# Performance work log

Measured on AMD Instinct MI355X. Metric: run time of the kernel, lower is better.

## Reference

```python
import jax, jax.numpy as jnp
import numpy as np

NEG_INF = -9e15
ALPHA = 0.2  # attention leaky_relu slope


def _gat_layer(h, adj_mask, W, a1, a2):
    # h: [N, Fin], W: [Fin, D], a1/a2: [D]
    Wh = h @ W                                   # [N, D]
    f1 = Wh @ a1                                 # [N]
    f2 = Wh @ a2                                 # [N]
    e = jax.nn.leaky_relu(f1[:, None] + f2[None, :], ALPHA)  # [N, N]
    scores = jnp.where(adj_mask, e, NEG_INF)
    att = jax.nn.softmax(scores, axis=-1)        # row-normalized over neighbors
    return att @ Wh                              # [N, D]


def setup_inputs() -> dict:
    key = jax.random.key(0)
    ks = jax.random.split(key, 12)
    N, Fin, H, D, C = 4096, 512, 8, 64, 64
    s = 0.1
    x = jax.random.normal(ks[0], (N, Fin), jnp.float32)
    adj = jax.random.randint(ks[1], (N, N), 0, 2, jnp.int32)
    W = jax.random.normal(ks[2], (H, Fin, D), jnp.float32) * s
    a1 = jax.random.normal(ks[3], (H, D), jnp.float32) * s
    a2 = jax.random.normal(ks[4], (H, D), jnp.float32) * s
    Wo = jax.random.normal(ks[5], (H * D, C), jnp.float32) * s
    ao1 = jax.random.normal(ks[6], (C,), jnp.float32) * s
    ao2 = jax.random.normal(ks[7], (C,), jnp.float32) * s
    W1 = jax.random.normal(ks[8], (512, N), jnp.float32) * 0.01  # nn.Linear(N, 512)
    b1 = jnp.zeros((512,), jnp.float32)
    W2 = jax.random.normal(ks[9], (256, 512), jnp.float32) * 0.04  # nn.Linear(512, 256)
    b2 = jnp.zeros((256,), jnp.float32)
    return {"x": x, "adj": adj, "W": W, "a1": a1, "a2": a2,
            "Wo": Wo, "ao1": ao1, "ao2": ao2,
            "W1": W1, "b1": b1, "W2": W2, "b2": b2}


def reference(x, adj, W, a1, a2, Wo, ao1, ao2, W1, b1, W2, b2):
    mask = adj > 0                                    # [N, N]
    # multi-head dense attention, concat=True -> ELU per head
    heads = jax.vmap(lambda Wk, a1k, a2k: _gat_layer(x, mask, Wk, a1k, a2k))(W, a1, a2)  # [H, N, D]
    h = jax.nn.elu(heads).transpose(1, 0, 2).reshape(x.shape[0], -1)  # [N, H*D]
    # output attention layer, concat=False (no inner ELU), then outer ELU
    out = jax.nn.elu(_gat_layer(h, mask, Wo, ao1, ao2))  # [N, C]
    out = jax.nn.log_softmax(out, axis=0)                # over nodes (dim=0)
    # MLP head on transposed features: [C, N] -> [C, 512] -> [C, 256]
    y = jax.nn.leaky_relu(out.T @ W1.T + b1, 0.1)
    y = y @ W2.T + b2
    return y
```

## Files before the change

### kernel.cpp

```cpp
#include <hip/hip_runtime.h>
#include <hip/hip_bf16.h>
#include <math.h>


#define N_NODES 4096
#define FIN 512
#define NHEAD 8
#define DHEAD 64
#define NCLS 64
#define NW 64

typedef unsigned short u16;
typedef unsigned long long u64;
typedef __attribute__((ext_vector_type(8))) short bf16x8;
typedef __attribute__((ext_vector_type(4))) float f32x4;

__device__ __forceinline__ float lrelu02(float x) { return x > 0.f ? x : 0.2f * x; }
__device__ __forceinline__ u16 bf16u(float x) {
    __hip_bfloat16 h = __float2bfloat16(x);
    return __builtin_bit_cast(unsigned short, h);
}
__device__ __forceinline__ f32x4 mfma16(bf16x8 a, bf16x8 b, f32x4 c) {
    return __builtin_amdgcn_mfma_f32_16x16x32_bf16(a, b, c, 0, 0, 0);
}
__device__ __forceinline__ unsigned fkey(float f) {
    unsigned u = __builtin_bit_cast(unsigned, f);
    return (u & 0x80000000u) ? ~u : (u | 0x80000000u);
}
__device__ __forceinline__ float funkey(unsigned k) {
    unsigned u = (k & 0x80000000u) ? (k ^ 0x80000000u) : ~k;
    return __builtin_bit_cast(float, u);
}

__global__ __launch_bounds__(256) void prep(
    const int* __restrict__ adj, u64* __restrict__ mb, unsigned* __restrict__ gmk,
    const float* __restrict__ x, u16* __restrict__ xB,
    const float* __restrict__ W1, u16* __restrict__ W1B,
    const float* __restrict__ W, const float* __restrict__ Wo,
    u16* __restrict__ WBt, u16* __restrict__ WoBt) {
    __shared__ alignas(16) u16 T[64][72];
    const int bid = blockIdx.x, t = threadIdx.x;
    if (bid < 1024) {
        if (bid == 0 && t < 16) gmk[t] = 0u;
        int nwaves = (1024 * 256) >> 6;
        int wid = (bid * 256 + t) >> 6;
        int lane = t & 63;
        for (int w = wid; w < N_NODES * NW; w += nwaves) {
            int i = w >> 6, wc = w & 63;
            int j = (wc << 6) | lane;
            u64 m = __ballot(adj[(size_t)i * N_NODES + j] > 0);
            if (lane == 0) mb[w] = m;
        }
    } else if (bid < 5120) {
        int i = (bid - 1024) * 256 + t;
        const float* s;
        u16* d;
        if (i < N_NODES * FIN / 4) { s = x; d = xB; }
        else { i -= N_NODES * FIN / 4; s = W1; d = W1B; }
        float4 v = ((const float4*)s)[i];
        ushort4 o = {bf16u(v.x), bf16u(v.y), bf16u(v.z), bf16u(v.w)};
        ((ushort4*)d)[i] = o;
    } else {
        int idx = bid - 5120;
        int y = idx >> 3, xb = idx & 7;
        const float* src = (y < 8) ? W + (size_t)y * FIN * DHEAD : Wo;
        u16* d = (y < 8) ? WBt + (size_t)y * DHEAD * FIN : WoBt;
        const int j0 = xb * 64;
        const int row = t & 63, g = t >> 6;
        #pragma unroll
        for (int k = 0; k < 16; k += 4) {
            float4 v = *(const float4*)(src + (size_t)(j0 + row) * 64 + g * 16 + k);
            T[g * 16 + k + 0][row] = bf16u(v.x);
            T[g * 16 + k + 1][row] = bf16u(v.y);
            T[g * 16 + k + 2][row] = bf16u(v.z);
            T[g * 16 + k + 3][row] = bf16u(v.w);
        }
        __syncthreads();
        const int dd = t >> 2, jc = (t & 3) * 16;
        *(uint4*)(d + (size_t)dd * FIN + j0 + jc) = *(const uint4*)&T[dd][jc];
        *(uint4*)(d + (size_t)dd * FIN + j0 + jc + 8) = *(const uint4*)&T[dd][jc + 8];
    }
}

__global__ __launch_bounds__(256) void gemm_fused(
    const u16* __restrict__ A, int lda, const u16* __restrict__ Bt, int ldb,
    const float* __restrict__ a1a, const float* __restrict__ a2a,
    u16* __restrict__ WhBT, float* __restrict__ f1o, float* __restrict__ f2o,
    unsigned* __restrict__ gmk, int K) {
    __shared__ alignas(16) u16 T[64][72];
    const int t = threadIdx.x, lane = t & 63, wv = t >> 6;
    const int c16 = lane & 15, kg = lane >> 4;
    const int h = blockIdx.x;
    const int bm = blockIdx.y * 64;
    const u16* Ap = A + (size_t)(bm + wv * 16 + c16) * lda + kg * 8;
    const u16* Bp = Bt + (size_t)(h * 64 + c16) * ldb + kg * 8;
    f32x4 acc[4] = {};
    #pragma unroll 4
    for (int k0 = 0; k0 < K; k0 += 32) {
        bf16x8 a = *(const bf16x8*)(Ap + k0);
        #pragma unroll
        for (int ct = 0; ct < 4; ++ct) {
            bf16x8 b = *(const bf16x8*)(Bp + (size_t)ct * 16 * ldb + k0);
            acc[ct] = mfma16(a, b, acc[ct]);
        }
    }
    float a1v[4], a2v[4];
    #pragma unroll
    for (int ct = 0; ct < 4; ++ct) {
        a1v[ct] = a1a[h * 64 + ct * 16 + c16];
        a2v[ct] = a2a[h * 64 + ct * 16 + c16];
    }
    float mx = -1e30f;
    #pragma unroll
    for (int r = 0; r < 4; ++r) {
        float s1 = 0.f, s2 = 0.f;
        int rl = wv * 16 + kg * 4 + r;
        #pragma unroll
        for (int ct = 0; ct < 4; ++ct) {
            float v = acc[ct][r];
            s1 = fmaf(v, a1v[ct], s1);
            s2 = fmaf(v, a2v[ct], s2);
            T[ct * 16 + c16][rl] = bf16u(v);
        }
        #pragma unroll
        for (int off = 1; off < 16; off <<= 1) {
            s1 += __shfl_xor(s1, off, 64);
            s2 += __shfl_xor(s2, off, 64);
        }
        if (c16 == 0) {
            f1o[(size_t)h * N_NODES + bm + rl] = s1;
            f2o[(size_t)h * N_NODES + bm + rl] = s2;
        }
        mx = fmaxf(mx, s2);
    }
    mx = fmaxf(mx, __shfl_xor(mx, 16, 64));
    mx = fmaxf(mx, __shfl_xor(mx, 32, 64));
    if (lane == 0) atomicMax(&gmk[h], fkey(mx));
    __syncthreads();
    const int dd = t >> 2, jc = (t & 3) * 16;
    u16* dst = WhBT + (size_t)(h * 64 + dd) * N_NODES + bm;
    *(uint4*)(dst + jc) = *(const uint4*)&T[dd][jc];
    *(uint4*)(dst + jc + 8) = *(const uint4*)&T[dd][jc + 8];
}

__global__ void coefk(const float* __restrict__ f1, const float* __restrict__ f2,
                      const unsigned* __restrict__ gmk, float4* __restrict__ rowc,
                      float2* __restrict__ uv) {
    int h = blockIdx.y;
    int i = blockIdx.x * 256 + threadIdx.x;
    float g = funkey(gmk[h]);
    float a = f1[(size_t)h * N_NODES + i];
    float s = a + g;
    float M = lrelu02(s);
    rowc[(size_t)h * N_NODES + i] = make_float4(__expf(s - M), __expf(0.2f * s - M), 0.f, 0.f);
    float b = f2[(size_t)h * N_NODES + i] - g;
    uv[(size_t)h * N_NODES + i] = make_float2(__expf(b), __expf(0.2f * b));
}

template <int NH, int ROWS, int JSPLIT, int OUTF>
__global__ __launch_bounds__(256) void attn_v3(
    const u16* __restrict__ WhB, const float2* __restrict__ uv,
    const float4* __restrict__ rowc, const u64* __restrict__ mb,
    float* __restrict__ outp, float* __restrict__ denP) {
    constexpr int NQ = ROWS / 4;
    constexpr int NMT = ROWS / 16;
    constexpr int NJT = (N_NODES / 64) / JSPLIT;
    __shared__ alignas(16) u16 pS[2][ROWS][64];
    __shared__ float Tof[(OUTF == 3) ? 64 * (ROWS + 1) : 1];
    const int b = blockIdx.x;
    int h, ib, js;
    if (NH == 8) { h = b & 7; int r = b >> 3; js = r % JSPLIT; ib = r / JSPLIT; }
    else { h = 0; js = b % JSPLIT; ib = b / JSPLIT; }
    const int i0 = ib * ROWS;
    const int jt0 = js * NJT;
    const int t = threadIdx.x, lane = t & 63, wv = t >> 6;
    const int wv_u = __builtin_amdgcn_readfirstlane(wv);

    const float2* __restrict__ uvp = uv + (size_t)h * N_NODES;
    const float4* __restrict__ rcp = rowc + (size_t)h * N_NODES;
    const u64* __restrict__ mbp = mb + (size_t)(i0 + wv_u) * NW + jt0;

    float Aq[NQ], Bq[NQ], den[NQ];
    #pragma unroll
    for (int q = 0; q < NQ; ++q) {
        float4 rc = rcp[i0 + q * 4 + wv];
        Aq[q] = rc.x; Bq[q] = rc.y; den[q] = 0.f;
    }
    const int wcE = lane ^ (wv << 3);
    const int wcO = lane ^ ((wv + 4) << 3);
    const int kg = lane >> 4, c16 = lane & 15;
    const int ocol = wv * 16 + c16;
    const u16* bptr = WhB + ((size_t)h * 64 + ocol) * N_NODES + jt0 * 64 + kg * 8;
    const int sw8 = (c16 & 7) << 3;
    f32x4 acc[NMT] = {};

    bf16x8 b0 = *(const bf16x8*)(bptr);
    bf16x8 b1 = *(const bf16x8*)(bptr + 32);
    float2 uvv = uvp[jt0 * 64 + lane];
    u64 m[NQ];
    #pragma unroll
    for (int q = 0; q < NQ; ++q) m[q] = mbp[q * 4 * NW];

    for (int it = 0; it < NJT; ++it) {
        const int buf = it & 1;
        const int nit = (it + 1 < NJT) ? it + 1 : it;
        bf16x8 nb0 = *(const bf16x8*)(bptr + (size_t)nit * 64);
        bf16x8 nb1 = *(const bf16x8*)(bptr + (size_t)nit * 64 + 32);
        float2 nuv = uvp[(jt0 + nit) * 64 + lane];
        u64 nm[NQ];
        #pragma unroll
        for (int q = 0; q < NQ; ++q) nm[q] = mbp[q * 4 * NW + nit];
        #pragma unroll
        for (int q = 0; q < NQ; ++q) {
            unsigned wlo = __builtin_amdgcn_readfirstlane((unsigned)m[q]);
            unsigned whi = __builtin_amdgcn_readfirstlane((unsigned)(m[q] >> 32));
            u64 ws = ((u64)whi << 32) | wlo;
            float tv = fmaxf(Aq[q] * uvv.x, Bq[q] * uvv.y);
            float p;
            asm("v_cndmask_b32 %0, 0, %1, %2" : "=v"(p) : "v"(tv), "s"(ws));
            den[q] += p;
            pS[buf][q * 4 + wv][(q & 1) ? wcO : wcE] = bf16u(p);
        }
        __syncthreads();
        __builtin_amdgcn_s_setprio(1);
        #pragma unroll
        for (int mt = 0; mt < NMT; ++mt) {
            const u16* ap = &pS[buf][mt * 16 + c16][0];
            bf16x8 a0 = *(const bf16x8*)&ap[(kg * 8) ^ sw8];
            bf16x8 a1 = *(const bf16x8*)&ap[(32 + kg * 8) ^ sw8];
            acc[mt] = mfma16(a0, b0, acc[mt]);
            acc[mt] = mfma16(a1, b1, acc[mt]);
        }
        __builtin_amdgcn_s_setprio(0);
        b0 = nb0; b1 = nb1; uvv = nuv;
        #pragma unroll
        for (int q = 0; q < NQ; ++q) m[q] = nm[q];
    }

    #pragma unroll
    for (int q = 0; q < NQ; ++q) {
        float s = den[q];
        #pragma unroll
        for (int off = 32; off; off >>= 1) s += __shfl_xor(s, off, 64);
        den[q] = s;
    }

    if constexpr (OUTF == 1) {
        if (lane == 0) {
            #pragma unroll
            for (int q = 0; q < NQ; ++q)
                denP[(size_t)js * (8 * N_NODES) + (size_t)h * N_NODES + i0 + q * 4 + wv] = den[q];
        }
        float* dst = outp + (size_t)js * N_NODES * 512;
        #pragma unroll
        for (int mt = 0; mt < NMT; ++mt)
            #pragma unroll
            for (int r = 0; r < 4; ++r)
                dst[(size_t)(i0 + mt * 16 + kg * 4 + r) * 512 + h * 64 + ocol] = acc[mt][r];
    } else {
        if (lane == 0) {
            #pragma unroll
            for (int q = 0; q < NQ; ++q)
                denP[(size_t)js * N_NODES + i0 + q * 4 + wv] = den[q];
        }
        #pragma unroll
        for (int mt = 0; mt < NMT; ++mt)
            #pragma unroll
            for (int r = 0; r < 4; ++r)
                Tof[ocol * (ROWS + 1) + mt * 16 + kg * 4 + r] = acc[mt][r];
        __syncthreads();
        const int c = t >> 2, r0 = (t & 3) * 8;
        float* dst = outp + (size_t)js * 64 * N_NODES + (size_t)c * N_NODES + i0 + r0;
        float4 v0 = {Tof[c * (ROWS + 1) + r0 + 0], Tof[c * (ROWS + 1) + r0 + 1],
                     Tof[c * (ROWS + 1) + r0 + 2], Tof[c * (ROWS + 1) + r0 + 3]};
        float4 v1 = {Tof[c * (ROWS + 1) + r0 + 4], Tof[c * (ROWS + 1) + r0 + 5],
                     Tof[c * (ROWS + 1) + r0 + 6], Tof[c * (ROWS + 1) + r0 + 7]};
        *(float4*)(dst) = v0;
        *(float4*)(dst + 4) = v1;
    }
}

__global__ __launch_bounds__(256) void combine8(
    const float* __restrict__ part, const float* __restrict__ denp,
    u16* __restrict__ hB) {
    const int t4 = (blockIdx.x * 256 + threadIdx.x) * 4;
    const int i = t4 >> 9, c = t4 & 511, h = c >> 6;
    float4 p0 = *(const float4*)(part + t4);
    float4 p1 = *(const float4*)(part + (size_t)N_NODES * 512 + t4);
    float d = denp[h * N_NODES + i] + denp[8 * N_NODES + h * N_NODES + i];
    float inv = d > 0.f ? 1.f / d : 0.f;
    float v[4] = {(p0.x + p1.x) * inv, (p0.y + p1.y) * inv,
                  (p0.z + p1.z) * inv, (p0.w + p1.w) * inv};
    ushort4 o;
    #pragma unroll
    for (int k = 0; k < 4; ++k) {
        float e = v[k] > 0.f ? v[k] : expm1f(v[k]);
        ((u16*)&o)[k] = bf16u(e);
    }
    *(ushort4*)(hB + t4) = o;
}

__global__ __launch_bounds__(256) void combine1_lsm(
    const float* __restrict__ partT, const float* __restrict__ denp,
    u16* __restrict__ lsT) {
    __shared__ float vb[N_NODES];
    __shared__ float r[256];
    const int c = blockIdx.x, t = threadIdx.x;
    float m = -1e30f;
    for (int i = t * 4; i < N_NODES; i += 1024) {
        float4 s = {0.f, 0.f, 0.f, 0.f}, d = {0.f, 0.f, 0.f, 0.f};
        #pragma unroll
        for (int js = 0; js < 4; ++js) {
            float4 pv = *(const float4*)(partT + (size_t)js * 64 * N_NODES +
                                         (size_t)c * N_NODES + i);
            float4 dv = *(const float4*)(denp + (size_t)js * N_NODES + i);
            s.x += pv.x; s.y += pv.y; s.z += pv.z; s.w += pv.w;
            d.x += dv.x; d.y += dv.y; d.z += dv.z; d.w += dv.w;
        }
        float vv[4] = {d.x > 0.f ? s.x / d.x : 0.f, d.y > 0.f ? s.y / d.y : 0.f,
                       d.z > 0.f ? s.z / d.z : 0.f, d.w > 0.f ? s.w / d.w : 0.f};
        #pragma unroll
        for (int k = 0; k < 4; ++k) {
            float e = vv[k] > 0.f ? vv[k] : expm1f(vv[k]);
            vb[i + k] = e;
            m = fmaxf(m, e);
        }
    }
    r[t] = m;
    __syncthreads();
    for (int s = 128; s; s >>= 1) {
        if (t < s) r[t] = fmaxf(r[t], r[t + s]);
        __syncthreads();
    }
    m = r[0];
    __syncthreads();
    float sum = 0.f;
    for (int i = t; i < N_NODES; i += 256) sum += __expf(vb[i] - m);
    r[t] = sum;
    __syncthreads();
    for (int s = 128; s; s >>= 1) {
        if (t < s) r[t] += r[t + s];
        __syncthreads();
    }
    float lse = m + __logf(r[0]);
    for (int i = t * 4; i < N_NODES; i += 1024) {
        ushort4 o = {bf16u(vb[i] - lse), bf16u(vb[i + 1] - lse),
                     bf16u(vb[i + 2] - lse), bf16u(vb[i + 3] - lse)};
        *(ushort4*)(lsT + (size_t)c * N_NODES + i) = o;
    }
}

__global__ __launch_bounds__(256) void mlp1_mfma(
    const u16* __restrict__ lsT, const u16* __restrict__ W1B,
    float* __restrict__ part) {
    const int t = threadIdx.x, lane = t & 63, wv = t >> 6;
    const int c16 = lane & 15, kg = lane >> 4;
    const int ks = blockIdx.x & 15;
    const int bn = (blockIdx.x >> 4) * 64;
    const int kb = ks * 256;
    const u16* Ap = lsT + (size_t)(wv * 16 + c16) * N_NODES + kb + kg * 8;
    const u16* Bp = W1B + (size_t)(bn + c16) * N_NODES + kb + kg * 8;
    f32x4 acc[4] = {};
    #pragma unroll
    for (int k0 = 0; k0 < 256; k0 += 32) {
        bf16x8 a = *(const bf16x8*)(Ap + k0);
        #pragma unroll
        for (int ct = 0; ct < 4; ++ct) {
            bf16x8 b = *(const bf16x8*)(Bp + (size_t)ct * 16 * N_NODES + k0);
            acc[ct] = mfma16(a, b, acc[ct]);
        }
    }
    float* dst = part + (size_t)ks * 64 * 512;
    #pragma unroll
    for (int ct = 0; ct < 4; ++ct)
        #pragma unroll
        for (int r = 0; r < 4; ++r)
            dst[(size_t)(wv * 16 + kg * 4 + r) * 512 + bn + ct * 16 + c16] = acc[ct][r];
}

__global__ __launch_bounds__(256) void mlp2f(
    const float* __restrict__ part, const float* __restrict__ b1,
    const float* __restrict__ W2, const float* __restrict__ b2,
    float* __restrict__ out) {
    __shared__ alignas(16) float row[512];
    const int c = blockIdx.x, t = threadIdx.x;
    #pragma unroll
    for (int half = 0; half < 2; ++half) {
        int o = t + half * 256;
        float s = 0.f;
        #pragma unroll
        for (int ks = 0; ks < 16; ++ks)
            s += part[(size_t)ks * 32768 + (size_t)c * 512 + o];
        s += b1[o];
        row[o] = s > 0.f ? s : 0.1f * s;
    }
    __syncthreads();
    float acc = 0.f;
    #pragma unroll 4
    for (int o = 0; o < 512; o += 4) {
        float4 w4 = *(const float4*)(W2 + (size_t)t * 512 + o);
        float4 r4 = *(const float4*)(&row[o]);
        acc += w4.x * r4.x + w4.y * r4.y + w4.z * r4.z + w4.w * r4.w;
    }
    out[(size_t)c * 256 + t] = acc + b2[t];
}

extern "C" void kernel_launch(void* const* d_in, const int* in_sizes, int n_in,
                              void* d_out, int out_size, void* d_ws, size_t ws_size,
                              hipStream_t stream) {
    const float* x   = (const float*)d_in[0];
    const int*   adj = (const int*)d_in[1];
    const float* W   = (const float*)d_in[2];
    const float* a1  = (const float*)d_in[3];
    const float* a2  = (const float*)d_in[4];
    const float* Wo  = (const float*)d_in[5];
    const float* ao1 = (const float*)d_in[6];
    const float* ao2 = (const float*)d_in[7];
    const float* W1  = (const float*)d_in[8];
    const float* b1  = (const float*)d_in[9];
    const float* W2  = (const float*)d_in[10];
    const float* b2  = (const float*)d_in[11];
    float* out = (float*)d_out;

    char* ws = (char*)d_ws;
    size_t off = 0;
    auto alloc = [&](size_t bytes) {
        void* p = ws + off;
        off += (bytes + 255) & ~(size_t)255;
        return p;
    };
    u64*     mb     = (u64*)alloc((size_t)N_NODES * NW * 8);
    u16*     xB     = (u16*)alloc((size_t)N_NODES * FIN * 2);
    u16*     WBt    = (u16*)alloc((size_t)NHEAD * DHEAD * FIN * 2);
    u16*     WoBt   = (u16*)alloc((size_t)DHEAD * FIN * 2);
    u16*     W1B    = (u16*)alloc((size_t)512 * N_NODES * 2);
    u16*     WhB    = (u16*)alloc((size_t)NHEAD * DHEAD * N_NODES * 2);
    u16*     WhoB   = (u16*)alloc((size_t)DHEAD * N_NODES * 2);
    u16*     hB     = (u16*)alloc((size_t)N_NODES * 512 * 2);
    float*   part8  = (float*)alloc((size_t)2 * N_NODES * 512 * 4);
    float*   den8   = (float*)alloc((size_t)2 * 8 * N_NODES * 4);
    float*   f1b    = (float*)alloc((size_t)9 * N_NODES * 4);
    float*   f2b    = (float*)alloc((size_t)9 * N_NODES * 4);
    unsigned* gmk   = (unsigned*)alloc(16 * 4);
    float4*  rowc   = (float4*)alloc((size_t)9 * N_NODES * 16);
    float2*  uvb    = (float2*)alloc((size_t)9 * N_NODES * 8);
    char*    ov     = (char*)part8;
    float*   partT1 = (float*)(ov);
    float*   den1   = (float*)(ov + ((size_t)4 << 20));
    u16*     lsT    = (u16*)(ov + ((size_t)4 << 20) + (256 << 10));
    float*   part   = (float*)(ov + ((size_t)5 << 20));
    (void)ws_size; (void)in_sizes; (void)n_in; (void)out_size;

    prep<<<5192, 256, 0, stream>>>(adj, mb, gmk, x, xB, W1, W1B, W, Wo, WBt, WoBt);
    gemm_fused<<<dim3(8, 64), 256, 0, stream>>>(xB, FIN, WBt, FIN, a1, a2,
                                                WhB, f1b, f2b, gmk, FIN);
    coefk<<<dim3(16, 8), 256, 0, stream>>>(f1b, f2b, gmk, rowc, uvb);
    attn_v3<8, 64, 2, 1><<<(N_NODES / 64) * 2 * 8, 256, 0, stream>>>(
        WhB, uvb, rowc, mb, part8, den8);
    combine8<<<N_NODES * 512 / 4 / 256, 256, 0, stream>>>(part8, den8, hB);
    gemm_fused<<<dim3(1, 64), 256, 0, stream>>>(hB, 512, WoBt, FIN, ao1, ao2,
                                                WhoB, f1b + (size_t)8 * N_NODES,
                                                f2b + (size_t)8 * N_NODES, gmk + 8, FIN);
    coefk<<<dim3(16, 1), 256, 0, stream>>>(f1b + (size_t)8 * N_NODES,
                                           f2b + (size_t)8 * N_NODES, gmk + 8,
                                           rowc + (size_t)8 * N_NODES,
                                           uvb + (size_t)8 * N_NODES);
    attn_v3<1, 32, 4, 3><<<(N_NODES / 32) * 4, 256, 0, stream>>>(
        WhoB, uvb + (size_t)8 * N_NODES, rowc + (size_t)8 * N_NODES, mb, partT1, den1);
    combine1_lsm<<<64, 256, 0, stream>>>(partT1, den1, lsT);
    mlp1_mfma<<<128, 256, 0, stream>>>(lsT, W1B, part);
    mlp2f<<<64, 256, 0, stream>>>(part, b1, W2, b2, out);
}
```

Baseline: 201.4 us.

## Unroll attention loop by two, store head partials in bf16, split output layer wider

The attention main loop is unrolled by two with named A/B register sets, so prefetches of the next tile's Wh, uv and mask words are interleaved explicitly with the P-fill and MFMA phases. The multi-head partial outputs are now stored as bf16 instead of fp32, which halves the write and read traffic between attn_v3 and combine8. The output-layer attention uses JSPLIT 8 instead of 4 to launch more blocks, and the workspace is enlarged into a 16MB pool to hold the extra partials. In exchange, the bf16 partial sums lose precision, and NJT must now be even for the unrolled loop to be correct (it is 32 and 8 here).

After: 217.2 us. +7.8%, slower.

```diff
diff --git a/kernel.cpp b/kernel.cpp
--- a/kernel.cpp
+++ b/kernel.cpp
@@ -19,6 +19,10 @@
 __device__ __forceinline__ u16 bf16u(float x) {
     __hip_bfloat16 h = __float2bfloat16(x);
     return __builtin_bit_cast(unsigned short, h);
+}
+__device__ __forceinline__ float b2f(u16 v) {
+    unsigned u = (unsigned)v << 16;
+    return __builtin_bit_cast(float, u);
 }
 __device__ __forceinline__ f32x4 mfma16(bf16x8 a, bf16x8 b, f32x4 c) {
     return __builtin_amdgcn_mfma_f32_16x16x32_bf16(a, b, c, 0, 0, 0);
@@ -161,7 +165,7 @@
 __global__ __launch_bounds__(256) void attn_v3(
     const u16* __restrict__ WhB, const float2* __restrict__ uv,
     const float4* __restrict__ rowc, const u64* __restrict__ mb,
-    float* __restrict__ outp, float* __restrict__ denP) {
+    void* __restrict__ outp, float* __restrict__ denP) {
     constexpr int NQ = ROWS / 4;
     constexpr int NMT = ROWS / 16;
     constexpr int NJT = (N_NODES / 64) / JSPLIT;
@@ -194,47 +198,60 @@
     const int sw8 = (c16 & 7) << 3;
     f32x4 acc[NMT] = {};
 
-    bf16x8 b0 = *(const bf16x8*)(bptr);
-    bf16x8 b1 = *(const bf16x8*)(bptr + 32);
-    float2 uvv = uvp[jt0 * 64 + lane];
-    u64 m[NQ];
-    #pragma unroll
-    for (int q = 0; q < NQ; ++q) m[q] = mbp[q * 4 * NW];
-
-    for (int it = 0; it < NJT; ++it) {
-        const int buf = it & 1;
-        const int nit = (it + 1 < NJT) ? it + 1 : it;
-        bf16x8 nb0 = *(const bf16x8*)(bptr + (size_t)nit * 64);
-        bf16x8 nb1 = *(const bf16x8*)(bptr + (size_t)nit * 64 + 32);
-        float2 nuv = uvp[(jt0 + nit) * 64 + lane];
-        u64 nm[NQ];
-        #pragma unroll
-        for (int q = 0; q < NQ; ++q) nm[q] = mbp[q * 4 * NW + nit];
+    bf16x8 bA0, bA1, bB0, bB1;
+    float2 uvA, uvB;
+    u64 mA[NQ], mB[NQ];
+
+    auto pfB = [&](int nit, bf16x8& x0, bf16x8& x1, float2& u) {
+        x0 = *(const bf16x8*)(bptr + (size_t)nit * 64);
+        x1 = *(const bf16x8*)(bptr + (size_t)nit * 64 + 32);
+        u = uvp[(jt0 + nit) * 64 + lane];
+    };
+    auto pfM = [&](int nit, u64* mm) {
+        #pragma unroll
+        for (int q = 0; q < NQ; ++q) mm[q] = mbp[q * 4 * NW + nit];
+    };
+    auto pph = [&](int bufI, const u64* mm, float2 u) {
         #pragma unroll
         for (int q = 0; q < NQ; ++q) {
-            unsigned wlo = __builtin_amdgcn_readfirstlane((unsigned)m[q]);
-            unsigned whi = __builtin_amdgcn_readfirstlane((unsigned)(m[q] >> 32));
+            unsigned wlo = __builtin_amdgcn_readfirstlane((unsigned)mm[q]);
+            unsigned whi = __builtin_amdgcn_readfirstlane((unsigned)(mm[q] >> 32));
             u64 ws = ((u64)whi << 32) | wlo;
-            float tv = fmaxf(Aq[q] * uvv.x, Bq[q] * uvv.y);
+            float tv = fmaxf(Aq[q] * u.x, Bq[q] * u.y);
             float p;
             asm("v_cndmask_b32 %0, 0, %1, %2" : "=v"(p) : "v"(tv), "s"(ws));
             den[q] += p;
-            pS[buf][q * 4 + wv][(q & 1) ? wcO : wcE] = bf16u(p);
-        }
-        __syncthreads();
+            pS[bufI][q * 4 + wv][(q & 1) ? wcO : wcE] = bf16u(p);
+        }
+    };
+    auto mm8 = [&](int bufI, bf16x8 v0, bf16x8 v1) {
         __builtin_amdgcn_s_setprio(1);
         #pragma unroll
         for (int mt = 0; mt < NMT; ++mt) {
-            const u16* ap = &pS[buf][mt * 16 + c16][0];
+            const u16* ap = &pS[bufI][mt * 16 + c16][0];
             bf16x8 a0 = *(const bf16x8*)&ap[(kg * 8) ^ sw8];
             bf16x8 a1 = *(const bf16x8*)&ap[(32 + kg * 8) ^ sw8];
-            acc[mt] = mfma16(a0, b0, acc[mt]);
-            acc[mt] = mfma16(a1, b1, acc[mt]);
+            acc[mt] = mfma16(a0, v0, acc[mt]);
+            acc[mt] = mfma16(a1, v1, acc[mt]);
         }
         __builtin_amdgcn_s_setprio(0);
-        b0 = nb0; b1 = nb1; uvv = nuv;
-        #pragma unroll
-        for (int q = 0; q < NQ; ++q) m[q] = nm[q];
+    };
+
+    pfB(0, bA0, bA1, uvA);
+    pfM(0, mA);
+    for (int it = 0; it < NJT; it += 2) {
+        const int itB = it + 1;
+        const int itC = (it + 2 < NJT) ? it + 2 : it;
+        pfB(itB, bB0, bB1, uvB);
+        pfM(itB, mB);
+        pph(0, mA, uvA);
+        __syncthreads();
+        mm8(0, bA0, bA1);
+        pfB(itC, bA0, bA1, uvA);
+        pfM(itC, mA);
+        pph(1, mB, uvB);
+        __syncthreads();
+        mm8(1, bB0, bB1);
     }
 
     #pragma unroll
@@ -251,12 +268,13 @@
             for (int q = 0; q < NQ; ++q)
                 denP[(size_t)js * (8 * N_NODES) + (size_t)h * N_NODES + i0 + q * 4 + wv] = den[q];
         }
-        float* dst = outp + (size_t)js * N_NODES * 512;
+        u16* dst = (u16*)outp + (size_t)js * N_NODES * 512;
         #pragma unroll
         for (int mt = 0; mt < NMT; ++mt)
             #pragma unroll
             for (int r = 0; r < 4; ++r)
-                dst[(size_t)(i0 + mt * 16 + kg * 4 + r) * 512 + h * 64 + ocol] = acc[mt][r];
+                dst[(size_t)(i0 + mt * 16 + kg * 4 + r) * 512 + h * 64 + ocol] =
+                    bf16u(acc[mt][r]);
     } else {
         if (lane == 0) {
             #pragma unroll
@@ -270,7 +288,7 @@
                 Tof[ocol * (ROWS + 1) + mt * 16 + kg * 4 + r] = acc[mt][r];
         __syncthreads();
         const int c = t >> 2, r0 = (t & 3) * 8;
-        float* dst = outp + (size_t)js * 64 * N_NODES + (size_t)c * N_NODES + i0 + r0;
+        float* dst = (float*)outp + (size_t)js * 64 * N_NODES + (size_t)c * N_NODES + i0 + r0;
         float4 v0 = {Tof[c * (ROWS + 1) + r0 + 0], Tof[c * (ROWS + 1) + r0 + 1],
                      Tof[c * (ROWS + 1) + r0 + 2], Tof[c * (ROWS + 1) + r0 + 3]};
         float4 v1 = {Tof[c * (ROWS + 1) + r0 + 4], Tof[c * (ROWS + 1) + r0 + 5],
@@ -281,16 +299,16 @@
 }
 
 __global__ __launch_bounds__(256) void combine8(
-    const float* __restrict__ part, const float* __restrict__ denp,
+    const u16* __restrict__ part, const float* __restrict__ denp,
     u16* __restrict__ hB) {
     const int t4 = (blockIdx.x * 256 + threadIdx.x) * 4;
     const int i = t4 >> 9, c = t4 & 511, h = c >> 6;
-    float4 p0 = *(const float4*)(part + t4);
-    float4 p1 = *(const float4*)(part + (size_t)N_NODES * 512 + t4);
+    ushort4 p0 = *(const ushort4*)(part + t4);
+    ushort4 p1 = *(const ushort4*)(part + (size_t)N_NODES * 512 + t4);
     float d = denp[h * N_NODES + i] + denp[8 * N_NODES + h * N_NODES + i];
     float inv = d > 0.f ? 1.f / d : 0.f;
-    float v[4] = {(p0.x + p1.x) * inv, (p0.y + p1.y) * inv,
-                  (p0.z + p1.z) * inv, (p0.w + p1.w) * inv};
+    float v[4] = {(b2f(p0.x) + b2f(p1.x)) * inv, (b2f(p0.y) + b2f(p1.y)) * inv,
+                  (b2f(p0.z) + b2f(p1.z)) * inv, (b2f(p0.w) + b2f(p1.w)) * inv};
     ushort4 o;
     #pragma unroll
     for (int k = 0; k < 4; ++k) {
@@ -310,7 +328,7 @@
     for (int i = t * 4; i < N_NODES; i += 1024) {
         float4 s = {0.f, 0.f, 0.f, 0.f}, d = {0.f, 0.f, 0.f, 0.f};
         #pragma unroll
-        for (int js = 0; js < 4; ++js) {
+        for (int js = 0; js < 8; ++js) {
             float4 pv = *(const float4*)(partT + (size_t)js * 64 * N_NODES +
                                          (size_t)c * N_NODES + i);
             float4 dv = *(const float4*)(denp + (size_t)js * N_NODES + i);
@@ -437,18 +455,18 @@
     u16*     WhB    = (u16*)alloc((size_t)NHEAD * DHEAD * N_NODES * 2);
     u16*     WhoB   = (u16*)alloc((size_t)DHEAD * N_NODES * 2);
     u16*     hB     = (u16*)alloc((size_t)N_NODES * 512 * 2);
-    float*   part8  = (float*)alloc((size_t)2 * N_NODES * 512 * 4);
+    char*    pool   = (char*)alloc((size_t)16 << 20);
     float*   den8   = (float*)alloc((size_t)2 * 8 * N_NODES * 4);
     float*   f1b    = (float*)alloc((size_t)9 * N_NODES * 4);
     float*   f2b    = (float*)alloc((size_t)9 * N_NODES * 4);
     unsigned* gmk   = (unsigned*)alloc(16 * 4);
     float4*  rowc   = (float4*)alloc((size_t)9 * N_NODES * 16);
     float2*  uvb    = (float2*)alloc((size_t)9 * N_NODES * 8);
-    char*    ov     = (char*)part8;
-    float*   partT1 = (float*)(ov);
-    float*   den1   = (float*)(ov + ((size_t)4 << 20));
-    u16*     lsT    = (u16*)(ov + ((size_t)4 << 20) + (256 << 10));
-    float*   part   = (float*)(ov + ((size_t)5 << 20));
+    u16*     part8  = (u16*)pool;
+    float*   partT1 = (float*)pool;
+    float*   den1   = (float*)(pool + ((size_t)8 << 20));
+    u16*     lsT    = (u16*)(pool + ((size_t)8 << 20) + (256 << 10));
+    float*   part   = (float*)(pool + ((size_t)9 << 20));
     (void)ws_size; (void)in_sizes; (void)n_in; (void)out_size;
 
     prep<<<5192, 256, 0, stream>>>(adj, mb, gmk, x, xB, W1, W1B, W, Wo, WBt, WoBt);
@@ -465,7 +483,7 @@
                                            f2b + (size_t)8 * N_NODES, gmk + 8,
                                            rowc + (size_t)8 * N_NODES,
                                            uvb + (size_t)8 * N_NODES);
-    attn_v3<1, 32, 4, 3><<<(N_NODES / 32) * 4, 256, 0, stream>>>(
+    attn_v3<1, 32, 8, 3><<<(N_NODES / 32) * 8, 256, 0, stream>>>(
         WhoB, uvb + (size_t)8 * N_NODES, rowc + (size_t)8 * N_NODES, mb, partT1, den1);
     combine1_lsm<<<64, 256, 0, stream>>>(partT1, den1, lsT);
     mlp1_mfma<<<128, 256, 0, stream>>>(lsT, W1B, part);
```

## Store head-layer partials in bf16, double output-layer J split, drop readfirstlane

Applied to the files above, without the earlier changes.

The multi-head attention kernel now writes its split-K partial accumulators as bf16 rather than fp32, halving the write and read traffic between attn_v3 and combine8. The output-layer attention is split eight ways along the neighbor dimension instead of four, which launches more blocks on the single-head stage, and its combine kernel sums eight partials. The mask word is passed straight to v_cndmask as an SGPR operand without explicit readfirstlane calls. The workspace is reorganized into a pool so the larger partT1 buffer fits. Rounding partial sums to bf16 before normalization adds precision loss.

New measurement: 204.1 us, median of 3. No clear change (+1.4%).

```diff
diff --git a/kernel.cpp b/kernel.cpp
--- a/kernel.cpp
+++ b/kernel.cpp
@@ -19,6 +19,10 @@
 __device__ __forceinline__ u16 bf16u(float x) {
     __hip_bfloat16 h = __float2bfloat16(x);
     return __builtin_bit_cast(unsigned short, h);
+}
+__device__ __forceinline__ float b2f(u16 v) {
+    unsigned u = (unsigned)v << 16;
+    return __builtin_bit_cast(float, u);
 }
 __device__ __forceinline__ f32x4 mfma16(bf16x8 a, bf16x8 b, f32x4 c) {
     return __builtin_amdgcn_mfma_f32_16x16x32_bf16(a, b, c, 0, 0, 0);
@@ -161,7 +165,7 @@
 __global__ __launch_bounds__(256) void attn_v3(
     const u16* __restrict__ WhB, const float2* __restrict__ uv,
     const float4* __restrict__ rowc, const u64* __restrict__ mb,
-    float* __restrict__ outp, float* __restrict__ denP) {
+    void* __restrict__ outp, float* __restrict__ denP) {
     constexpr int NQ = ROWS / 4;
     constexpr int NMT = ROWS / 16;
     constexpr int NJT = (N_NODES / 64) / JSPLIT;
@@ -212,12 +216,9 @@
         for (int q = 0; q < NQ; ++q) nm[q] = mbp[q * 4 * NW + nit];
         #pragma unroll
         for (int q = 0; q < NQ; ++q) {
-            unsigned wlo = __builtin_amdgcn_readfirstlane((unsigned)m[q]);
-            unsigned whi = __builtin_amdgcn_readfirstlane((unsigned)(m[q] >> 32));
-            u64 ws = ((u64)whi << 32) | wlo;
             float tv = fmaxf(Aq[q] * uvv.x, Bq[q] * uvv.y);
             float p;
-            asm("v_cndmask_b32 %0, 0, %1, %2" : "=v"(p) : "v"(tv), "s"(ws));
+            asm("v_cndmask_b32 %0, 0, %1, %2" : "=v"(p) : "v"(tv), "s"(m[q]));
             den[q] += p;
             pS[buf][q * 4 + wv][(q & 1) ? wcO : wcE] = bf16u(p);
         }
@@ -251,12 +252,13 @@
             for (int q = 0; q < NQ; ++q)
                 denP[(size_t)js * (8 * N_NODES) + (size_t)h * N_NODES + i0 + q * 4 + wv] = den[q];
         }
-        float* dst = outp + (size_t)js * N_NODES * 512;
+        u16* dst = (u16*)outp + (size_t)js * N_NODES * 512;
         #pragma unroll
         for (int mt = 0; mt < NMT; ++mt)
             #pragma unroll
             for (int r = 0; r < 4; ++r)
-                dst[(size_t)(i0 + mt * 16 + kg * 4 + r) * 512 + h * 64 + ocol] = acc[mt][r];
+                dst[(size_t)(i0 + mt * 16 + kg * 4 + r) * 512 + h * 64 + ocol] =
+                    bf16u(acc[mt][r]);
     } else {
         if (lane == 0) {
             #pragma unroll
@@ -270,7 +272,7 @@
                 Tof[ocol * (ROWS + 1) + mt * 16 + kg * 4 + r] = acc[mt][r];
         __syncthreads();
         const int c = t >> 2, r0 = (t & 3) * 8;
-        float* dst = outp + (size_t)js * 64 * N_NODES + (size_t)c * N_NODES + i0 + r0;
+        float* dst = (float*)outp + (size_t)js * 64 * N_NODES + (size_t)c * N_NODES + i0 + r0;
         float4 v0 = {Tof[c * (ROWS + 1) + r0 + 0], Tof[c * (ROWS + 1) + r0 + 1],
                      Tof[c * (ROWS + 1) + r0 + 2], Tof[c * (ROWS + 1) + r0 + 3]};
         float4 v1 = {Tof[c * (ROWS + 1) + r0 + 4], Tof[c * (ROWS + 1) + r0 + 5],
@@ -281,16 +283,16 @@
 }
 
 __global__ __launch_bounds__(256) void combine8(
-    const float* __restrict__ part, const float* __restrict__ denp,
+    const u16* __restrict__ part, const float* __restrict__ denp,
     u16* __restrict__ hB) {
     const int t4 = (blockIdx.x * 256 + threadIdx.x) * 4;
     const int i = t4 >> 9, c = t4 & 511, h = c >> 6;
-    float4 p0 = *(const float4*)(part + t4);
-    float4 p1 = *(const float4*)(part + (size_t)N_NODES * 512 + t4);
+    ushort4 p0 = *(const ushort4*)(part + t4);
+    ushort4 p1 = *(const ushort4*)(part + (size_t)N_NODES * 512 + t4);
     float d = denp[h * N_NODES + i] + denp[8 * N_NODES + h * N_NODES + i];
     float inv = d > 0.f ? 1.f / d : 0.f;
-    float v[4] = {(p0.x + p1.x) * inv, (p0.y + p1.y) * inv,
-                  (p0.z + p1.z) * inv, (p0.w + p1.w) * inv};
+    float v[4] = {(b2f(p0.x) + b2f(p1.x)) * inv, (b2f(p0.y) + b2f(p1.y)) * inv,
+                  (b2f(p0.z) + b2f(p1.z)) * inv, (b2f(p0.w) + b2f(p1.w)) * inv};
     ushort4 o;
     #pragma unroll
     for (int k = 0; k < 4; ++k) {
@@ -310,7 +312,7 @@
     for (int i = t * 4; i < N_NODES; i += 1024) {
         float4 s = {0.f, 0.f, 0.f, 0.f}, d = {0.f, 0.f, 0.f, 0.f};
         #pragma unroll
-        for (int js = 0; js < 4; ++js) {
+        for (int js = 0; js < 8; ++js) {
             float4 pv = *(const float4*)(partT + (size_t)js * 64 * N_NODES +
                                          (size_t)c * N_NODES + i);
             float4 dv = *(const float4*)(denp + (size_t)js * N_NODES + i);
@@ -437,18 +439,18 @@
     u16*     WhB    = (u16*)alloc((size_t)NHEAD * DHEAD * N_NODES * 2);
     u16*     WhoB   = (u16*)alloc((size_t)DHEAD * N_NODES * 2);
     u16*     hB     = (u16*)alloc((size_t)N_NODES * 512 * 2);
-    float*   part8  = (float*)alloc((size_t)2 * N_NODES * 512 * 4);
+    char*    pool   = (char*)alloc((size_t)16 << 20);
     float*   den8   = (float*)alloc((size_t)2 * 8 * N_NODES * 4);
     float*   f1b    = (float*)alloc((size_t)9 * N_NODES * 4);
     float*   f2b    = (float*)alloc((size_t)9 * N_NODES * 4);
     unsigned* gmk   = (unsigned*)alloc(16 * 4);
     float4*  rowc   = (float4*)alloc((size_t)9 * N_NODES * 16);
     float2*  uvb    = (float2*)alloc((size_t)9 * N_NODES * 8);
-    char*    ov     = (char*)part8;
-    float*   partT1 = (float*)(ov);
-    float*   den1   = (float*)(ov + ((size_t)4 << 20));
-    u16*     lsT    = (u16*)(ov + ((size_t)4 << 20) + (256 << 10));
-    float*   part   = (float*)(ov + ((size_t)5 << 20));
+    u16*     part8  = (u16*)pool;
+    float*   partT1 = (float*)pool;
+    float*   den1   = (float*)(pool + ((size_t)8 << 20));
+    u16*     lsT    = (u16*)(pool + ((size_t)8 << 20) + (256 << 10));
+    float*   part   = (float*)(pool + ((size_t)9 << 20));
     (void)ws_size; (void)in_sizes; (void)n_in; (void)out_size;
 
     prep<<<5192, 256, 0, stream>>>(adj, mb, gmk, x, xB, W1, W1B, W, Wo, WBt, WoBt);
@@ -465,7 +467,7 @@
                                            f2b + (size_t)8 * N_NODES, gmk + 8,
                                            rowc + (size_t)8 * N_NODES,
                                            uvb + (size_t)8 * N_NODES);
-    attn_v3<1, 32, 4, 3><<<(N_NODES / 32) * 4, 256, 0, stream>>>(
+    attn_v3<1, 32, 8, 3><<<(N_NODES / 32) * 8, 256, 0, stream>>>(
         WhoB, uvb + (size_t)8 * N_NODES, rowc + (size_t)8 * N_NODES, mb, partT1, den1);
     combine1_lsm<<<64, 256, 0, stream>>>(partT1, den1, lsT);
     mlp1_mfma<<<128, 256, 0, stream>>>(lsT, W1B, part);
```
